# Kernel tuning notes

Hardware: AMD Instinct MI355X
Metric: run time of the kernel (lower is better)

## Reference

```python
import jax, jax.numpy as jnp
import numpy as np

N_PDE = 4096
SENSOR_RANGE = 0.08
WINDOW = int(SENSOR_RANGE * N_PDE)   # 327
HALF = WINDOW // 2                   # 163
RESIZE_LEN = 20
FREQS = jnp.array([1.0, 2.0, 4.0, 8.0], dtype=jnp.float32)
EPS = 1e-6  # flax GroupNorm default epsilon
U_MAX, V_MAX = 40.0, 1.0
N_AGENTS = 262144


def setup_inputs() -> dict:
    key = jax.random.key(0)
    ks = jax.random.split(key, 16)

    def w(k, shape):
        fan_in = shape[0]
        return (jax.random.normal(k, shape, jnp.float32) / np.float32(np.sqrt(fan_in)))

    return {
        "z_curr": jax.random.normal(ks[0], (N_PDE,), jnp.float32),
        "z_target": jax.random.normal(ks[1], (N_PDE,), jnp.float32),
        "xi_curr": jax.random.uniform(ks[2], (N_AGENTS,), jnp.float32),
        # branch net (features=[256,256]), each layer: Dense + GroupNorm(1 group) + tanh
        "bW0": w(ks[3], (2 * RESIZE_LEN, 256)), "bb0": jnp.zeros((256,), jnp.float32),
        "bs0": jnp.ones((256,), jnp.float32), "bB0": jnp.zeros((256,), jnp.float32),
        "bW1": w(ks[4], (256, 256)), "bb1": jnp.zeros((256,), jnp.float32),
        "bs1": jnp.ones((256,), jnp.float32), "bB1": jnp.zeros((256,), jnp.float32),
        # trunk net: 8 -> 32 -> 32
        "tW0": w(ks[5], (8, 32)), "tb0": jnp.zeros((32,), jnp.float32),
        "tW1": w(ks[6], (32, 32)), "tb1": jnp.zeros((32,), jnp.float32),
        # combined head: (256+32) -> 32, then two 32 -> 1 heads
        "cW": w(ks[7], (256 + 32, 32)), "cb": jnp.zeros((32,), jnp.float32),
        "uW": w(ks[8], (32, 1)), "ub": jnp.zeros((1,), jnp.float32),
        "vW": w(ks[9], (32, 1)), "vb": jnp.zeros((1,), jnp.float32),
    }


def _local_obs(padded_error, xi):
    # per-agent dynamic slice + finite-difference gradient + bilinear resize
    center = (xi * (N_PDE - 1)).astype(jnp.int32) + HALF
    start = center - HALF
    p_err = jax.lax.dynamic_slice(padded_error, (start,), (WINDOW,))
    p_grad = jnp.gradient(p_err)
    p_err = jax.image.resize(p_err, (RESIZE_LEN,), method='bilinear')
    p_grad = jax.image.resize(p_grad, (RESIZE_LEN,), method='bilinear')
    return jnp.concatenate([p_err, p_grad])  # [40]


def _groupnorm1(x, scale, bias):
    # GroupNorm(num_groups=1) applied per-sample over the feature axis
    mu = jnp.mean(x, axis=-1, keepdims=True)
    var = jnp.var(x, axis=-1, keepdims=True)
    return (x - mu) * jax.lax.rsqrt(var + EPS) * scale + bias


def reference(z_curr, z_target, xi_curr,
              bW0, bb0, bs0, bB0, bW1, bb1, bs1, bB1,
              tW0, tb0, tW1, tb1, cW, cb, uW, ub, vW, vb):
    error = z_curr - z_target
    padded = jnp.pad(error, (HALF, HALF), mode='edge')  # [N_PDE + 2*HALF]

    patches = jax.vmap(lambda xi: _local_obs(padded, xi))(xi_curr)  # [A, 40]

    # branch net
    h = jnp.tanh(_groupnorm1(patches @ bW0 + bb0, bs0, bB0))  # [A, 256]
    h = jnp.tanh(_groupnorm1(h @ bW1 + bb1, bs1, bB1))        # [A, 256]

    # trunk net
    angle = xi_curr[:, None] * FREQS * jnp.pi                 # [A, 4]
    enc = jnp.concatenate([jnp.sin(angle), jnp.cos(angle)], axis=-1)  # [A, 8]
    enc = jnp.tanh(enc @ tW0 + tb0)
    enc = jnp.tanh(enc @ tW1 + tb1)                           # [A, 32]

    combined = jnp.concatenate([h, enc], axis=-1)             # [A, 288]
    x = jnp.tanh(combined @ cW + cb)                          # [A, 32]
    u_raw = (x @ uW + ub).squeeze(-1)
    v_raw = (x @ vW + vb).squeeze(-1)
    return (U_MAX * jnp.tanh(u_raw), V_MAX * jnp.tanh(v_raw))
```

## Files before the change

### kernel.cpp

```cpp
#include <hip/hip_runtime.h>

#define NP      4096
#define WINDOW  327
#define HALF    163
#define RL      20
#define NA      262144
#define GN_EPS  1e-6f
#define R       8
#define NBLK    (NP / R)

__device__ __forceinline__ float tanh_fast(float x) {
  float e = __expf(2.0f * x);
  return 1.0f - 2.0f / (e + 1.0f);
}

__device__ __forceinline__ void halfwave_sum2(float& a, float& b) {
#pragma unroll
  for (int m = 1; m < 32; m <<= 1) {
    a += __shfl_xor(a, m, 64);
    b += __shfl_xor(b, m, 64);
  }
}

#define L_ESP   0
#define L_OBS   336
#define L_HBUF  656
#define L_PART  2736
#define L_HCL   10928
#define L_TOT   11216

__global__ __launch_bounds__(256, 2) void dc_table(
    const float* __restrict__ zc,  const float* __restrict__ zt,
    const float* __restrict__ bW0, const float* __restrict__ bb0,
    const float* __restrict__ bs0, const float* __restrict__ bB0,
    const float* __restrict__ bW1, const float* __restrict__ bb1,
    const float* __restrict__ bs1, const float* __restrict__ bB1,
    const float* __restrict__ tW0, const float* __restrict__ tb0,
    const float* __restrict__ tW1, const float* __restrict__ tb1,
    const float* __restrict__ cW,  const float* __restrict__ cb,
    const float* __restrict__ uW,  const float* __restrict__ ub,
    const float* __restrict__ vW,  const float* __restrict__ vb,
    float* __restrict__ tbl)
{
  __shared__ __align__(16) float sm[L_TOT];
  float* espan = sm + L_ESP;
  float* obsT  = sm + L_OBS;
  float* hbuf  = sm + L_HBUF;
  float* part  = sm + L_PART;
  float* hcL   = sm + L_HCL;

  const int tid = threadIdx.x;
  const int w   = tid >> 6;
  const int l   = tid & 63;
  const int s0  = blockIdx.x * R;

  for (int t = tid; t < WINDOW + R - 1; t += 256) {
    int c = s0 - HALF + t;
    c = c < 0 ? 0 : (c > NP - 1 ? NP - 1 : c);
    espan[t] = zc[c] - zt[c];
  }
  __syncthreads();

  {
    const float INV  = (float)WINDOW / (float)RL;
    const float RINV = (float)RL / (float)WINDOW;
    for (int task = tid; task < R * 2 * RL; task += 256) {
      int q = task % (2 * RL);
      int r = task / (2 * RL);
      int qq = (q < RL) ? q : q - RL;
      float xs = ((float)qq + 0.5f) * INV - 0.5f;
      int jlo = (int)ceilf(xs - INV);  if (jlo < 0) jlo = 0;
      int jhi = (int)floorf(xs + INV); if (jhi > WINDOW - 1) jhi = WINDOW - 1;
      const float* p = espan + r;
      float wsum = 0.0f, acc = 0.0f;
      for (int j = jlo; j <= jhi; ++j) {
        float wq = 1.0f - fabsf(xs - (float)j) * RINV;
        float v;
        if (q < RL) {
          v = p[j];
        } else {
          v = (j == 0) ? (p[1] - p[0]) :
              (j == WINDOW - 1) ? (p[WINDOW - 1] - p[WINDOW - 2]) :
              0.5f * (p[j + 1] - p[j - 1]);
        }
        wsum += wq;
        acc  += wq * v;
      }
      obsT[q * 8 + r] = acc / wsum;
    }
  }
  __syncthreads();

  float acc[R][4];

#pragma unroll
  for (int r = 0; r < R; ++r) { acc[r][0]=0.f; acc[r][1]=0.f; acc[r][2]=0.f; acc[r][3]=0.f; }
#pragma unroll 2
  for (int kk = 0; kk < 10; ++kk) {
    int k = w * 10 + kk;
    float4 wt = *(const float4*)&bW0[k * 256 + 4 * l];
    float4 o0 = *(const float4*)&obsT[k * 8];
    float4 o1 = *(const float4*)&obsT[k * 8 + 4];
    const float wv[4] = {wt.x, wt.y, wt.z, wt.w};
    const float ov[8] = {o0.x, o0.y, o0.z, o0.w, o1.x, o1.y, o1.z, o1.w};
#pragma unroll
    for (int r = 0; r < R; ++r)
#pragma unroll
      for (int j = 0; j < 4; ++j) acc[r][j] = fmaf(ov[r], wv[j], acc[r][j]);
  }

  {
#pragma unroll
    for (int r = 0; r < R; ++r)
      *(float4*)&part[w * 2048 + r * 256 + 4 * l] = make_float4(acc[r][0], acc[r][1], acc[r][2], acc[r][3]);
    __syncthreads();
    int rr = tid >> 5, g = tid & 31;
    float val[8];
    {
      float4 b0 = *(const float4*)&bb0[8 * g];
      float4 b1 = *(const float4*)&bb0[8 * g + 4];
      val[0]=b0.x; val[1]=b0.y; val[2]=b0.z; val[3]=b0.w;
      val[4]=b1.x; val[5]=b1.y; val[6]=b1.z; val[7]=b1.w;
    }
#pragma unroll
    for (int w2 = 0; w2 < 4; ++w2) {
      float4 p0 = *(const float4*)&part[w2 * 2048 + rr * 256 + 8 * g];
      float4 p1 = *(const float4*)&part[w2 * 2048 + rr * 256 + 8 * g + 4];
      val[0]+=p0.x; val[1]+=p0.y; val[2]+=p0.z; val[3]+=p0.w;
      val[4]+=p1.x; val[5]+=p1.y; val[6]+=p1.z; val[7]+=p1.w;
    }
    float s = 0.f, q = 0.f;
#pragma unroll
    for (int i = 0; i < 8; ++i) { s += val[i]; q += val[i] * val[i]; }
    halfwave_sum2(s, q);
    float mu  = s * (1.0f / 256.0f);
    float var = fmaxf(q * (1.0f / 256.0f) - mu * mu, 0.0f);
    float rv  = rsqrtf(var + GN_EPS);
    float4 sc0 = *(const float4*)&bs0[8 * g];
    float4 sc1 = *(const float4*)&bs0[8 * g + 4];
    float4 sh0 = *(const float4*)&bB0[8 * g];
    float4 sh1 = *(const float4*)&bB0[8 * g + 4];
    const float sc[8] = {sc0.x,sc0.y,sc0.z,sc0.w,sc1.x,sc1.y,sc1.z,sc1.w};
    const float sh[8] = {sh0.x,sh0.y,sh0.z,sh0.w,sh1.x,sh1.y,sh1.z,sh1.w};
    float h[8];
#pragma unroll
    for (int i = 0; i < 8; ++i) h[i] = tanh_fast((val[i] - mu) * rv * sc[i] + sh[i]);
    *(float4*)&hbuf[rr * 260 + 8 * g]     = make_float4(h[0], h[1], h[2], h[3]);
    *(float4*)&hbuf[rr * 260 + 8 * g + 4] = make_float4(h[4], h[5], h[6], h[7]);
  }
  __syncthreads();

#pragma unroll
  for (int r = 0; r < R; ++r) { acc[r][0]=0.f; acc[r][1]=0.f; acc[r][2]=0.f; acc[r][3]=0.f; }
#pragma unroll 2
  for (int kk = 0; kk < 64; kk += 4) {
    int k0 = w * 64 + kk;
    float4 wt0 = *(const float4*)&bW1[(k0    ) * 256 + 4 * l];
    float4 wt1 = *(const float4*)&bW1[(k0 + 1) * 256 + 4 * l];
    float4 wt2 = *(const float4*)&bW1[(k0 + 2) * 256 + 4 * l];
    float4 wt3 = *(const float4*)&bW1[(k0 + 3) * 256 + 4 * l];
    float4 hr[R];
#pragma unroll
    for (int r = 0; r < R; ++r) hr[r] = *(const float4*)&hbuf[r * 260 + k0];
#pragma unroll
    for (int r = 0; r < R; ++r) {
      const float* hp = (const float*)&hr[r];
      acc[r][0] = fmaf(hp[0], wt0.x, acc[r][0]); acc[r][1] = fmaf(hp[0], wt0.y, acc[r][1]);
      acc[r][2] = fmaf(hp[0], wt0.z, acc[r][2]); acc[r][3] = fmaf(hp[0], wt0.w, acc[r][3]);
      acc[r][0] = fmaf(hp[1], wt1.x, acc[r][0]); acc[r][1] = fmaf(hp[1], wt1.y, acc[r][1]);
      acc[r][2] = fmaf(hp[1], wt1.z, acc[r][2]); acc[r][3] = fmaf(hp[1], wt1.w, acc[r][3]);
      acc[r][0] = fmaf(hp[2], wt2.x, acc[r][0]); acc[r][1] = fmaf(hp[2], wt2.y, acc[r][1]);
      acc[r][2] = fmaf(hp[2], wt2.z, acc[r][2]); acc[r][3] = fmaf(hp[2], wt2.w, acc[r][3]);
      acc[r][0] = fmaf(hp[3], wt3.x, acc[r][0]); acc[r][1] = fmaf(hp[3], wt3.y, acc[r][1]);
      acc[r][2] = fmaf(hp[3], wt3.z, acc[r][2]); acc[r][3] = fmaf(hp[3], wt3.w, acc[r][3]);
    }
  }

  {
#pragma unroll
    for (int r = 0; r < R; ++r)
      *(float4*)&part[w * 2048 + r * 256 + 4 * l] = make_float4(acc[r][0], acc[r][1], acc[r][2], acc[r][3]);
    __syncthreads();
    int rr = tid >> 5, g = tid & 31;
    float val[8];
    {
      float4 b0 = *(const float4*)&bb1[8 * g];
      float4 b1 = *(const float4*)&bb1[8 * g + 4];
      val[0]=b0.x; val[1]=b0.y; val[2]=b0.z; val[3]=b0.w;
      val[4]=b1.x; val[5]=b1.y; val[6]=b1.z; val[7]=b1.w;
    }
#pragma unroll
    for (int w2 = 0; w2 < 4; ++w2) {
      float4 p0 = *(const float4*)&part[w2 * 2048 + rr * 256 + 8 * g];
      float4 p1 = *(const float4*)&part[w2 * 2048 + rr * 256 + 8 * g + 4];
      val[0]+=p0.x; val[1]+=p0.y; val[2]+=p0.z; val[3]+=p0.w;
      val[4]+=p1.x; val[5]+=p1.y; val[6]+=p1.z; val[7]+=p1.w;
    }
    float s = 0.f, q = 0.f;
#pragma unroll
    for (int i = 0; i < 8; ++i) { s += val[i]; q += val[i] * val[i]; }
    halfwave_sum2(s, q);
    float mu  = s * (1.0f / 256.0f);
    float var = fmaxf(q * (1.0f / 256.0f) - mu * mu, 0.0f);
    float rv  = rsqrtf(var + GN_EPS);
    float4 sc0 = *(const float4*)&bs1[8 * g];
    float4 sc1 = *(const float4*)&bs1[8 * g + 4];
    float4 sh0 = *(const float4*)&bB1[8 * g];
    float4 sh1 = *(const float4*)&bB1[8 * g + 4];
    const float sc[8] = {sc0.x,sc0.y,sc0.z,sc0.w,sc1.x,sc1.y,sc1.z,sc1.w};
    const float sh[8] = {sh0.x,sh0.y,sh0.z,sh0.w,sh1.x,sh1.y,sh1.z,sh1.w};
    float h[8];
#pragma unroll
    for (int i = 0; i < 8; ++i) h[i] = tanh_fast((val[i] - mu) * rv * sc[i] + sh[i]);
    *(float4*)&hbuf[rr * 260 + 8 * g]     = make_float4(h[0], h[1], h[2], h[3]);
    *(float4*)&hbuf[rr * 260 + 8 * g + 4] = make_float4(h[4], h[5], h[6], h[7]);
  }
  __syncthreads();

  {
    int r = tid >> 5, c = tid & 31;
    float ga = cb[c];
#pragma unroll 4
    for (int k = 0; k < 256; k += 4) {
      float4 hv = *(const float4*)&hbuf[r * 260 + k];
      ga = fmaf(hv.x, cW[(k    ) * 32 + c], ga);
      ga = fmaf(hv.y, cW[(k + 1) * 32 + c], ga);
      ga = fmaf(hv.z, cW[(k + 2) * 32 + c], ga);
      ga = fmaf(hv.w, cW[(k + 3) * 32 + c], ga);
    }
    hcL[r * 36 + c] = ga;
  }
  __syncthreads();

  if (tid < 128) {
    int v = tid >> 3, sub = tid & 7;
    int r = v >> 1, e = v & 1;
    int jg = s0 + r + e;
    float xe = (float)jg * (1.0f / 4095.0f);
    float enc[8];
#pragma unroll
    for (int k = 0; k < 4; ++k) {
      float fr = (float)(1 << k);
      float a = (xe * fr) * 3.14159265358979f;
      enc[k]     = sinf(a);
      enc[k + 4] = cosf(a);
    }
    int base = (tid & 63) & ~7;

    float t0v[4];
#pragma unroll
    for (int i = 0; i < 4; ++i) {
      int f = 4 * sub + i;
      float a = tb0[f];
#pragma unroll
      for (int k = 0; k < 8; ++k) a = fmaf(enc[k], tW0[k * 32 + f], a);
      t0v[i] = tanh_fast(a);
    }

    float t1v[4];
#pragma unroll
    for (int i = 0; i < 4; ++i) t1v[i] = tb1[4 * sub + i];
#pragma unroll
    for (int j8 = 0; j8 < 8; ++j8) {
#pragma unroll
      for (int i2 = 0; i2 < 4; ++i2) {
        float tv = __shfl(t0v[i2], base + j8, 64);
        int k = 4 * j8 + i2;
#pragma unroll
        for (int i = 0; i < 4; ++i) t1v[i] = fmaf(tv, tW1[k * 32 + 4 * sub + i], t1v[i]);
      }
    }
#pragma unroll
    for (int i = 0; i < 4; ++i) t1v[i] = tanh_fast(t1v[i]);

    float xvv[4];
#pragma unroll
    for (int i = 0; i < 4; ++i) xvv[i] = hcL[r * 36 + 4 * sub + i];
#pragma unroll
    for (int j8 = 0; j8 < 8; ++j8) {
#pragma unroll
      for (int i2 = 0; i2 < 4; ++i2) {
        float tv = __shfl(t1v[i2], base + j8, 64);
        int k = 4 * j8 + i2;
#pragma unroll
        for (int i = 0; i < 4; ++i) xvv[i] = fmaf(tv, cW[(256 + k) * 32 + 4 * sub + i], xvv[i]);
      }
    }
#pragma unroll
    for (int i = 0; i < 4; ++i) xvv[i] = tanh_fast(xvv[i]);

    float up = 0.f, vp = 0.f;
#pragma unroll
    for (int i = 0; i < 4; ++i) {
      up = fmaf(xvv[i], uW[4 * sub + i], up);
      vp = fmaf(xvv[i], vW[4 * sub + i], vp);
    }
#pragma unroll
    for (int m = 1; m < 8; m <<= 1) {
      up += __shfl_xor(up, m, 64);
      vp += __shfl_xor(vp, m, 64);
    }
    if (sub == 0) {
      int s = s0 + r;
      tbl[4 * s + e]     = 40.0f * tanh_fast(up + ub[0]);
      tbl[4 * s + 2 + e] = tanh_fast(vp + vb[0]);
    }
  }
}

__global__ __launch_bounds__(256) void dc_agents(
    const float* __restrict__ xi_curr, const float4* __restrict__ tbl,
    float* __restrict__ out)
{
  int a = blockIdx.x * 256 + threadIdx.x;
  float xi = xi_curr[a];
  float p = xi * 4095.0f;
  int s = (int)p;
  s = s > 4095 ? 4095 : s;
  float t = p - (float)s;
  float4 tb = tbl[s];
  out[a]      = fmaf(t, tb.y - tb.x, tb.x);
  out[NA + a] = fmaf(t, tb.w - tb.z, tb.z);
}

extern "C" void kernel_launch(void* const* d_in, const int* in_sizes, int n_in,
                              void* d_out, int out_size, void* d_ws, size_t ws_size,
                              hipStream_t stream) {
  const float* zc  = (const float*)d_in[0];
  const float* zt  = (const float*)d_in[1];
  const float* xi  = (const float*)d_in[2];
  const float* bW0 = (const float*)d_in[3];
  const float* bb0 = (const float*)d_in[4];
  const float* bs0 = (const float*)d_in[5];
  const float* bB0 = (const float*)d_in[6];
  const float* bW1 = (const float*)d_in[7];
  const float* bb1 = (const float*)d_in[8];
  const float* bs1 = (const float*)d_in[9];
  const float* bB1 = (const float*)d_in[10];
  const float* tW0 = (const float*)d_in[11];
  const float* tb0 = (const float*)d_in[12];
  const float* tW1 = (const float*)d_in[13];
  const float* tb1 = (const float*)d_in[14];
  const float* cW  = (const float*)d_in[15];
  const float* cb  = (const float*)d_in[16];
  const float* uW  = (const float*)d_in[17];
  const float* ub  = (const float*)d_in[18];
  const float* vW  = (const float*)d_in[19];
  const float* vb  = (const float*)d_in[20];

  float* tbl = (float*)d_ws;
  float* out = (float*)d_out;

  dc_table<<<NBLK, 256, 0, stream>>>(zc, zt, bW0, bb0, bs0, bB0,
                                     bW1, bb1, bs1, bB1,
                                     tW0, tb0, tW1, tb1, cW, cb,
                                     uW, ub, vW, vb, tbl);
  dc_agents<<<NA / 256, 256, 0, stream>>>(xi, (const float4*)tbl, out);
}
```

Measured before the change: 130.0 us.

## Halve rows per block to raise occupancy and remap per-row work

Reduces the number of table rows each block processes from 8 to 4, doubling the grid. Shared memory use roughly halves and launch bounds now request 4 blocks per CU. The GroupNorm and head stages are remapped so each wave owns one row, with a full-wave reduction and a split-K cW dot product combined by a shuffle. Each block now loads the weight matrices for half as many rows, so total global weight traffic roughly doubles while more blocks can run at once.

```diff
diff --git a/kernel.cpp b/kernel.cpp
--- a/kernel.cpp
+++ b/kernel.cpp
@@ -6,7 +6,7 @@
 #define RL      20
 #define NA      262144
 #define GN_EPS  1e-6f
-#define R       8
+#define R       4
 #define NBLK    (NP / R)
 
 __device__ __forceinline__ float tanh_fast(float x) {
@@ -14,22 +14,22 @@
   return 1.0f - 2.0f / (e + 1.0f);
 }
 
-__device__ __forceinline__ void halfwave_sum2(float& a, float& b) {
-#pragma unroll
-  for (int m = 1; m < 32; m <<= 1) {
+__device__ __forceinline__ void wave_sum2(float& a, float& b) {
+#pragma unroll
+  for (int m = 1; m < 64; m <<= 1) {
     a += __shfl_xor(a, m, 64);
     b += __shfl_xor(b, m, 64);
   }
 }
 
 #define L_ESP   0
-#define L_OBS   336
-#define L_HBUF  656
-#define L_PART  2736
-#define L_HCL   10928
-#define L_TOT   11216
-
-__global__ __launch_bounds__(256, 2) void dc_table(
+#define L_OBS   332
+#define L_HBUF  492
+#define L_PART  1532
+#define L_HCL   5628
+#define L_TOT   5772
+
+__global__ __launch_bounds__(256, 4) void dc_table(
     const float* __restrict__ zc,  const float* __restrict__ zt,
     const float* __restrict__ bW0, const float* __restrict__ bb0,
     const float* __restrict__ bs0, const float* __restrict__ bB0,
@@ -64,7 +64,8 @@
   {
     const float INV  = (float)WINDOW / (float)RL;
     const float RINV = (float)RL / (float)WINDOW;
-    for (int task = tid; task < R * 2 * RL; task += 256) {
+    int task = tid;
+    if (task < R * 2 * RL) {
       int q = task % (2 * RL);
       int r = task / (2 * RL);
       int qq = (q < RL) ? q : q - RL;
@@ -86,7 +87,7 @@
         wsum += wq;
         acc  += wq * v;
       }
-      obsT[q * 8 + r] = acc / wsum;
+      obsT[q * 4 + r] = acc / wsum;
     }
   }
   __syncthreads();
@@ -99,10 +100,9 @@
   for (int kk = 0; kk < 10; ++kk) {
     int k = w * 10 + kk;
     float4 wt = *(const float4*)&bW0[k * 256 + 4 * l];
-    float4 o0 = *(const float4*)&obsT[k * 8];
-    float4 o1 = *(const float4*)&obsT[k * 8 + 4];
+    float4 o  = *(const float4*)&obsT[k * 4];
     const float wv[4] = {wt.x, wt.y, wt.z, wt.w};
-    const float ov[8] = {o0.x, o0.y, o0.z, o0.w, o1.x, o1.y, o1.z, o1.w};
+    const float ov[4] = {o.x, o.y, o.z, o.w};
 #pragma unroll
     for (int r = 0; r < R; ++r)
 #pragma unroll
@@ -112,41 +112,34 @@
   {
 #pragma unroll
     for (int r = 0; r < R; ++r)
-      *(float4*)&part[w * 2048 + r * 256 + 4 * l] = make_float4(acc[r][0], acc[r][1], acc[r][2], acc[r][3]);
+      *(float4*)&part[w * 1024 + r * 256 + 4 * l] = make_float4(acc[r][0], acc[r][1], acc[r][2], acc[r][3]);
     __syncthreads();
-    int rr = tid >> 5, g = tid & 31;
-    float val[8];
+    int rr = w, g = l;
+    float val[4];
     {
-      float4 b0 = *(const float4*)&bb0[8 * g];
-      float4 b1 = *(const float4*)&bb0[8 * g + 4];
+      float4 b0 = *(const float4*)&bb0[4 * g];
       val[0]=b0.x; val[1]=b0.y; val[2]=b0.z; val[3]=b0.w;
-      val[4]=b1.x; val[5]=b1.y; val[6]=b1.z; val[7]=b1.w;
     }
 #pragma unroll
     for (int w2 = 0; w2 < 4; ++w2) {
-      float4 p0 = *(const float4*)&part[w2 * 2048 + rr * 256 + 8 * g];
-      float4 p1 = *(const float4*)&part[w2 * 2048 + rr * 256 + 8 * g + 4];
+      float4 p0 = *(const float4*)&part[w2 * 1024 + rr * 256 + 4 * g];
       val[0]+=p0.x; val[1]+=p0.y; val[2]+=p0.z; val[3]+=p0.w;
-      val[4]+=p1.x; val[5]+=p1.y; val[6]+=p1.z; val[7]+=p1.w;
     }
     float s = 0.f, q = 0.f;
 #pragma unroll
-    for (int i = 0; i < 8; ++i) { s += val[i]; q += val[i] * val[i]; }
-    halfwave_sum2(s, q);
+    for (int i = 0; i < 4; ++i) { s += val[i]; q += val[i] * val[i]; }
+    wave_sum2(s, q);
     float mu  = s * (1.0f / 256.0f);
     float var = fmaxf(q * (1.0f / 256.0f) - mu * mu, 0.0f);
     float rv  = rsqrtf(var + GN_EPS);
-    float4 sc0 = *(const float4*)&bs0[8 * g];
-    float4 sc1 = *(const float4*)&bs0[8 * g + 4];
-    float4 sh0 = *(const float4*)&bB0[8 * g];
-    float4 sh1 = *(const float4*)&bB0[8 * g + 4];
-    const float sc[8] = {sc0.x,sc0.y,sc0.z,sc0.w,sc1.x,sc1.y,sc1.z,sc1.w};
-    const float sh[8] = {sh0.x,sh0.y,sh0.z,sh0.w,sh1.x,sh1.y,sh1.z,sh1.w};
-    float h[8];
-#pragma unroll
-    for (int i = 0; i < 8; ++i) h[i] = tanh_fast((val[i] - mu) * rv * sc[i] + sh[i]);
-    *(float4*)&hbuf[rr * 260 + 8 * g]     = make_float4(h[0], h[1], h[2], h[3]);
-    *(float4*)&hbuf[rr * 260 + 8 * g + 4] = make_float4(h[4], h[5], h[6], h[7]);
+    float4 sc0 = *(const float4*)&bs0[4 * g];
+    float4 sh0 = *(const float4*)&bB0[4 * g];
+    const float sc[4] = {sc0.x,sc0.y,sc0.z,sc0.w};
+    const float sh[4] = {sh0.x,sh0.y,sh0.z,sh0.w};
+    float h[4];
+#pragma unroll
+    for (int i = 0; i < 4; ++i) h[i] = tanh_fast((val[i] - mu) * rv * sc[i] + sh[i]);
+    *(float4*)&hbuf[rr * 260 + 4 * g] = make_float4(h[0], h[1], h[2], h[3]);
   }
   __syncthreads();
 
@@ -179,60 +172,56 @@
   {
 #pragma unroll
     for (int r = 0; r < R; ++r)
-      *(float4*)&part[w * 2048 + r * 256 + 4 * l] = make_float4(acc[r][0], acc[r][1], acc[r][2], acc[r][3]);
+      *(float4*)&part[w * 1024 + r * 256 + 4 * l] = make_float4(acc[r][0], acc[r][1], acc[r][2], acc[r][3]);
     __syncthreads();
-    int rr = tid >> 5, g = tid & 31;
-    float val[8];
+    int rr = w, g = l;
+    float val[4];
     {
-      float4 b0 = *(const float4*)&bb1[8 * g];
-      float4 b1 = *(const float4*)&bb1[8 * g + 4];
+      float4 b0 = *(const float4*)&bb1[4 * g];
       val[0]=b0.x; val[1]=b0.y; val[2]=b0.z; val[3]=b0.w;
-      val[4]=b1.x; val[5]=b1.y; val[6]=b1.z; val[7]=b1.w;
     }
 #pragma unroll
     for (int w2 = 0; w2 < 4; ++w2) {
-      float4 p0 = *(const float4*)&part[w2 * 2048 + rr * 256 + 8 * g];
-      float4 p1 = *(const float4*)&part[w2 * 2048 + rr * 256 + 8 * g + 4];
+      float4 p0 = *(const float4*)&part[w2 * 1024 + rr * 256 + 4 * g];
       val[0]+=p0.x; val[1]+=p0.y; val[2]+=p0.z; val[3]+=p0.w;
-      val[4]+=p1.x; val[5]+=p1.y; val[6]+=p1.z; val[7]+=p1.w;
     }
     float s = 0.f, q = 0.f;
 #pragma unroll
-    for (int i = 0; i < 8; ++i) { s += val[i]; q += val[i] * val[i]; }
-    halfwave_sum2(s, q);
+    for (int i = 0; i < 4; ++i) { s += val[i]; q += val[i] * val[i]; }
+    wave_sum2(s, q);
     float mu  = s * (1.0f / 256.0f);
     float var = fmaxf(q * (1.0f / 256.0f) - mu * mu, 0.0f);
     float rv  = rsqrtf(var + GN_EPS);
-    float4 sc0 = *(const float4*)&bs1[8 * g];
-    float4 sc1 = *(const float4*)&bs1[8 * g + 4];
-    float4 sh0 = *(const float4*)&bB1[8 * g];
-    float4 sh1 = *(const float4*)&bB1[8 * g + 4];
-    const float sc[8] = {sc0.x,sc0.y,sc0.z,sc0.w,sc1.x,sc1.y,sc1.z,sc1.w};
-    const float sh[8] = {sh0.x,sh0.y,sh0.z,sh0.w,sh1.x,sh1.y,sh1.z,sh1.w};
-    float h[8];
-#pragma unroll
-    for (int i = 0; i < 8; ++i) h[i] = tanh_fast((val[i] - mu) * rv * sc[i] + sh[i]);
-    *(float4*)&hbuf[rr * 260 + 8 * g]     = make_float4(h[0], h[1], h[2], h[3]);
-    *(float4*)&hbuf[rr * 260 + 8 * g + 4] = make_float4(h[4], h[5], h[6], h[7]);
+    float4 sc0 = *(const float4*)&bs1[4 * g];
+    float4 sh0 = *(const float4*)&bB1[4 * g];
+    const float sc[4] = {sc0.x,sc0.y,sc0.z,sc0.w};
+    const float sh[4] = {sh0.x,sh0.y,sh0.z,sh0.w};
+    float h[4];
+#pragma unroll
+    for (int i = 0; i < 4; ++i) h[i] = tanh_fast((val[i] - mu) * rv * sc[i] + sh[i]);
+    *(float4*)&hbuf[rr * 260 + 4 * g] = make_float4(h[0], h[1], h[2], h[3]);
   }
   __syncthreads();
 
   {
-    int r = tid >> 5, c = tid & 31;
-    float ga = cb[c];
+    int r = w;
+    int c = l & 31;
+    int kh = (l >> 5) * 128;
+    float ga = (l < 32) ? cb[c] : 0.0f;
 #pragma unroll 4
-    for (int k = 0; k < 256; k += 4) {
+    for (int k = kh; k < kh + 128; k += 4) {
       float4 hv = *(const float4*)&hbuf[r * 260 + k];
       ga = fmaf(hv.x, cW[(k    ) * 32 + c], ga);
       ga = fmaf(hv.y, cW[(k + 1) * 32 + c], ga);
       ga = fmaf(hv.z, cW[(k + 2) * 32 + c], ga);
       ga = fmaf(hv.w, cW[(k + 3) * 32 + c], ga);
     }
-    hcL[r * 36 + c] = ga;
-  }
-  __syncthreads();
-
-  if (tid < 128) {
+    ga += __shfl_xor(ga, 32, 64);
+    if (l < 32) hcL[r * 36 + c] = ga;
+  }
+  __syncthreads();
+
+  if (tid < 64) {
     int v = tid >> 3, sub = tid & 7;
     int r = v >> 1, e = v & 1;
     int jg = s0 + r + e;
@@ -245,7 +234,7 @@
       enc[k]     = sinf(a);
       enc[k + 4] = cosf(a);
     }
-    int base = (tid & 63) & ~7;
+    int base = tid & ~7;
 
     float t0v[4];
 #pragma unroll
```

Result: faster. 123.4 us (-5.1%).
